# Kernel tuning notes

Hardware: AMD Instinct MI355X
Metric: run time of the kernel (lower is better)

Reference implementation:

```python
import jax, jax.numpy as jnp
import numpy as np

C = 512
GROUPS = 8
EPS = 1e-5


def setup_inputs() -> dict:
    key = jax.random.key(0)
    ks = jax.random.split(key, 7)
    B, H, W = 16, 32, 32
    x = jax.random.normal(ks[0], (B, C, H, W), dtype=jnp.float32)
    gamma = jnp.ones((C,), jnp.float32)
    beta = jnp.zeros((C,), jnp.float32)
    # 1x1 convs stored as [out, in] matrices
    w_qkv = jax.random.normal(ks[1], (3 * C, C), dtype=jnp.float32) * (1.0 / np.sqrt(C))
    b_qkv = jax.random.normal(ks[2], (3 * C,), dtype=jnp.float32) * 0.02
    w_proj = jax.random.normal(ks[3], (C, C), dtype=jnp.float32) * (1.0 / np.sqrt(C))
    b_proj = jax.random.normal(ks[4], (C,), dtype=jnp.float32) * 0.02
    return {"x": x, "gamma": gamma, "beta": beta, "w_qkv": w_qkv,
            "b_qkv": b_qkv, "w_proj": w_proj, "b_proj": b_proj}


def _group_norm(x, gamma, beta):
    B, Cc, H, W = x.shape
    xg = x.reshape(B, GROUPS, Cc // GROUPS, H, W)
    mean = xg.mean(axis=(2, 3, 4), keepdims=True)
    var = xg.var(axis=(2, 3, 4), keepdims=True)
    xg = (xg - mean) * jax.lax.rsqrt(var + EPS)
    x = xg.reshape(B, Cc, H, W)
    return x * gamma[None, :, None, None] + beta[None, :, None, None]


def reference(x, gamma, beta, w_qkv, b_qkv, w_proj, b_proj):
    B, Cc, H, W = x.shape
    N = H * W
    h = _group_norm(x, gamma, beta)  # [B,C,H,W]
    hf = h.reshape(B, Cc, N)  # [B,C,N]
    # 1x1 conv == matmul over channel dim
    qkv = jnp.einsum('oc,bcn->bon', w_qkv, hf) + b_qkv[None, :, None]  # [B,3C,N]
    q, k, v = jnp.split(qkv, 3, axis=1)  # each [B,C,N]
    scale = 1.0 / jnp.sqrt(jnp.float32(Cc))
    # attn[b,i,j] = sum_c q[b,c,i] * k[b,c,j]
    attn = jnp.einsum('bci,bcj->bij', q, k) * scale  # [B,N,N]
    attn = jax.nn.softmax(attn, axis=-1)
    out = jnp.einsum('bij,bcj->bci', attn, v)  # [B,C,N]
    out = jnp.einsum('oc,bcn->bon', w_proj, out) + b_proj[None, :, None]
    return x + out.reshape(B, Cc, H, W)
```

## Files before the change

### kernel.cpp

```cpp
#include <hip/hip_runtime.h>
#include <hip/hip_bf16.h>

typedef unsigned short u16;
typedef unsigned int u32;
typedef __attribute__((ext_vector_type(8))) short short8;
typedef __attribute__((ext_vector_type(4))) float floatx4;

#define BATCH 16
#define CDIM 512
#define NSPAT 1024
#define NGROUP 8

__device__ __forceinline__ u16 f2bf(float f) {
    unsigned u = __float_as_uint(f);
    u += 0x7FFFu + ((u >> 16) & 1u);
    return (u16)(u >> 16);
}
__device__ __forceinline__ u32 f2bf2(float lo, float hi) {
    __hip_bfloat162 h = __float22bfloat162_rn(make_float2(lo, hi));
    return *(u32*)&h;
}

__device__ __forceinline__ void load_lds16(const void* g, void* l) {
    __builtin_amdgcn_global_load_lds(
        (const __attribute__((address_space(1))) unsigned int*)g,
        (__attribute__((address_space(3))) unsigned int*)l, 16, 0, 0);
}

__global__ __launch_bounds__(256) void prep_kernel(
    const float* __restrict__ w_qkv, const float* __restrict__ w_proj,
    const float* __restrict__ b_qkv, const float* __restrict__ x,
    u16* __restrict__ wmega, u16* __restrict__ wproj_bf, u16* __restrict__ wv_t,
    float* __restrict__ stats, float* __restrict__ lsums, float* __restrict__ bpv) {
    int b = blockIdx.x;
    int tid = threadIdx.x;
    if (b < 768) {
        const float* src = (b < 512) ? w_qkv : w_proj;
        u16* dst = (b < 512) ? wmega : wproj_bf;
        int i = (b < 512 ? b : b - 512) * 256 + tid;
        float4 v = ((const float4*)src)[i];
        u32* d = (u32*)dst;
        d[i * 2] = f2bf2(v.x, v.y);
        d[i * 2 + 1] = f2bf2(v.z, v.w);
        return;
    }
    if (b < 832) {
        __shared__ u16 t[64 * 66];
        int bt = b - 768;
        int tx = bt & 7, ty = bt >> 3;
        const float* src = w_qkv + (size_t)(1024 + ty * 64) * CDIM + tx * 64;
#pragma unroll
        for (int p = 0; p < 4; ++p) {
            int r = p * 16 + (tid >> 4);
            int c4 = (tid & 15) << 2;
            float4 v = *(const float4*)(src + (size_t)r * CDIM + c4);
            u16* d = &t[r * 66 + c4];
            d[0] = f2bf(v.x); d[1] = f2bf(v.y); d[2] = f2bf(v.z); d[3] = f2bf(v.w);
        }
        __syncthreads();
        u16* dst = wv_t + (size_t)(tx * 64) * CDIM + ty * 64;
#pragma unroll
        for (int p = 0; p < 4; ++p) {
            int c = p * 16 + (tid >> 4);
            int r4 = (tid & 15) << 2;
            ushort4 o;
            o.x = t[(r4 + 0) * 66 + c];
            o.y = t[(r4 + 1) * 66 + c];
            o.z = t[(r4 + 2) * 66 + c];
            o.w = t[(r4 + 3) * 66 + c];
            *(ushort4*)(dst + (size_t)c * CDIM + r4) = o;
        }
        return;
    }
    if (b < 960) {
        __shared__ float rs[4], rss[4];
        int bg = b - 832;
        const float4* xv = (const float4*)(x + (size_t)bg * 65536);
        float s = 0.f, ss = 0.f;
        for (int i = tid; i < 16384; i += 256) {
            float4 v = xv[i];
            s += v.x + v.y + v.z + v.w;
            ss += v.x * v.x + v.y * v.y + v.z * v.z + v.w * v.w;
        }
#pragma unroll
        for (int off = 32; off; off >>= 1) { s += __shfl_down(s, off); ss += __shfl_down(ss, off); }
        int wave = tid >> 6, lane = tid & 63;
        if (lane == 0) { rs[wave] = s; rss[wave] = ss; }
        __syncthreads();
        if (tid == 0) {
            float S1 = rs[0] + rs[1] + rs[2] + rs[3];
            float S2 = rss[0] + rss[1] + rss[2] + rss[3];
            float mean = S1 * (1.f / 65536.f);
            float var = S2 * (1.f / 65536.f) - mean * mean;
            stats[bg * 2] = mean;
            stats[bg * 2 + 1] = rsqrtf(var + 1e-5f);
        }
        return;
    }
    if (b < 976) {
        ((float4*)lsums)[(b - 960) * 256 + tid] = (float4){0.f, 0.f, 0.f, 0.f};
        return;
    }
    {
        int o0 = (b - 976) * 64;
        int wave = tid >> 6, lane = tid & 63;
        const float4* bvv = (const float4*)(b_qkv + 1024);
        float4 v0 = bvv[lane * 2], v1 = bvv[lane * 2 + 1];
        for (int it = 0; it < 16; ++it) {
            int o = o0 + wave * 16 + it;
            const float4* wr = (const float4*)(w_proj + (size_t)o * CDIM);
            float4 a0 = wr[lane * 2], a1 = wr[lane * 2 + 1];
            float s = a0.x * v0.x + a0.y * v0.y + a0.z * v0.z + a0.w * v0.w
                    + a1.x * v1.x + a1.y * v1.y + a1.z * v1.z + a1.w * v1.w;
#pragma unroll
            for (int off = 32; off; off >>= 1) s += __shfl_down(s, off);
            if (lane == 0) bpv[o] = s;
        }
    }
}

__device__ __forceinline__ void stage_tile(
    const u16* __restrict__ Ab, const u16* __restrict__ Bb, int lda, int ldb,
    int m0, int n0, int k0, u16* As, u16* Bs) {
    int tid = threadIdx.x;
#pragma unroll
    for (int it = 0; it < 4; ++it) {
        int c = it * 256 + tid;
        int r = c >> 3, p = c & 7;
        int kc = p ^ (r & 7);
        load_lds16(Ab + (size_t)(m0 + r) * lda + k0 + (kc << 3), &As[c << 3]);
        load_lds16(Bb + (size_t)(n0 + r) * ldb + k0 + (kc << 3), &Bs[c << 3]);
    }
}

__device__ __forceinline__ void compute_tile(
    const u16* As, const u16* Bs, int wm, int wn, int quad, int lrow,
    floatx4 (&acc)[4][4]) {
#pragma unroll
    for (int s = 0; s < 2; ++s) {
        short8 af[4], bf[4];
#pragma unroll
        for (int i = 0; i < 4; ++i) {
            int R = wm + i * 16 + lrow;
            int p = (s * 4 + quad) ^ (R & 7);
            af[i] = *(const short8*)&As[(R << 6) + (p << 3)];
        }
#pragma unroll
        for (int j = 0; j < 4; ++j) {
            int R = wn + j * 16 + lrow;
            int p = (s * 4 + quad) ^ (R & 7);
            bf[j] = *(const short8*)&Bs[(R << 6) + (p << 3)];
        }
#pragma unroll
        for (int i = 0; i < 4; ++i)
#pragma unroll
            for (int j = 0; j < 4; ++j)
                acc[i][j] = __builtin_amdgcn_mfma_f32_16x16x32_bf16(af[i], bf[j], acc[i][j], 0, 0, 0);
    }
}

template <bool DB>
__device__ __forceinline__ void gemm_core(
    const u16* __restrict__ Ab, const u16* __restrict__ Bb, int K, int lda, int ldb,
    int m0, int n0, u16* As, u16* Bs, floatx4 (&acc)[4][4]) {
    int tid = threadIdx.x;
    int lane = tid & 63, wave = tid >> 6, quad = lane >> 4, lrow = lane & 15;
    int wm = (wave >> 1) << 6, wn = (wave & 1) << 6;
    if constexpr (!DB) {
        for (int k0 = 0; k0 < K; k0 += 64) {
            stage_tile(Ab, Bb, lda, ldb, m0, n0, k0, As, Bs);
            __syncthreads();
            compute_tile(As, Bs, wm, wn, quad, lrow, acc);
            __syncthreads();
        }
    } else {
        const int TS = 128 * 64;
        int nt = K >> 6;
        stage_tile(Ab, Bb, lda, ldb, m0, n0, 0, As, Bs);
        u16 *Ac = As, *Bc = Bs, *An = As + TS, *Bn = Bs + TS;
        for (int t = 0; t < nt - 1; ++t) {
            stage_tile(Ab, Bb, lda, ldb, m0, n0, (t + 1) << 6, An, Bn);
            asm volatile("s_waitcnt vmcnt(8)" ::: "memory");
            __builtin_amdgcn_s_barrier();
            __builtin_amdgcn_sched_barrier(0);
            compute_tile(Ac, Bc, wm, wn, quad, lrow, acc);
            __builtin_amdgcn_sched_barrier(0);
            __builtin_amdgcn_s_barrier();
            u16* t0 = Ac; Ac = An; An = t0;
            u16* t1 = Bc; Bc = Bn; Bn = t1;
        }
        asm volatile("s_waitcnt vmcnt(0)" ::: "memory");
        __builtin_amdgcn_s_barrier();
        __builtin_amdgcn_sched_barrier(0);
        compute_tile(Ac, Bc, wm, wn, quad, lrow, acc);
    }
}

#define ACC_INIT floatx4 acc[4][4]; \
    _Pragma("unroll") for (int i = 0; i < 4; ++i) \
    _Pragma("unroll") for (int j = 0; j < 4; ++j) acc[i][j] = (floatx4){0.f, 0.f, 0.f, 0.f};

#define EPILOG_IDX int lane = threadIdx.x & 63, wave = threadIdx.x >> 6; \
    int quad = lane >> 4, lrow = lane & 15; \
    int wm = (wave >> 1) << 6, wn = (wave & 1) << 6;

#define TSTR 66
__global__ __launch_bounds__(256) void gn_wpv_kernel(
    const float* __restrict__ x, const float* __restrict__ gamma, const float* __restrict__ beta,
    const float* __restrict__ stats, u16* __restrict__ hT,
    const u16* __restrict__ wproj_bf, const u16* __restrict__ wv_t, u16* __restrict__ wmega) {
    __shared__ u16 smem[2 * 128 * 64];
    int tid = threadIdx.x;
    if (blockIdx.z == 16) {
        if (blockIdx.x >= 4 || blockIdx.y >= 4) return;
        int m0 = blockIdx.y << 7, n0 = blockIdx.x << 7;
        ACC_INIT;
        gemm_core<false>(wproj_bf, wv_t, CDIM, CDIM, CDIM, m0, n0, smem, smem + 128 * 64, acc);
        EPILOG_IDX;
#pragma unroll
        for (int i = 0; i < 4; ++i)
#pragma unroll
            for (int j = 0; j < 4; ++j)
#pragma unroll
                for (int r = 0; r < 4; ++r) {
                    int R = m0 + wm + i * 16 + (quad << 2) + r;
                    int Cc = n0 + wn + j * 16 + lrow;
                    wmega[(size_t)(1024 + R) * CDIM + Cc] = f2bf(acc[i][j][r]);
                }
        return;
    }
    u16* t = smem;
    int b = blockIdx.z, c0 = blockIdx.y << 6, n0 = blockIdx.x << 6;
    const float* xb = x + ((size_t)b * CDIM + c0) * NSPAT + n0;
#pragma unroll
    for (int p = 0; p < 4; ++p) {
        int cl = p * 16 + (tid >> 4);
        int nl = (tid & 15) << 2;
        int c = c0 + cl;
        int bg = b * NGROUP + (c >> 6);
        float ga = gamma[c] * stats[bg * 2 + 1];
        float be = beta[c] - stats[bg * 2] * ga;
        float4 v = *(const float4*)(xb + (size_t)cl * NSPAT + nl);
        u16* dst = &t[cl * TSTR + nl];
        dst[0] = f2bf(v.x * ga + be);
        dst[1] = f2bf(v.y * ga + be);
        dst[2] = f2bf(v.z * ga + be);
        dst[3] = f2bf(v.w * ga + be);
    }
    __syncthreads();
    u16* hb = hT + ((size_t)b * NSPAT + n0) * CDIM + c0;
#pragma unroll
    for (int p = 0; p < 4; ++p) {
        int nl = p * 16 + (tid >> 4);
        int cl4 = (tid & 15) << 2;
        ushort4 o;
        o.x = t[(cl4 + 0) * TSTR + nl];
        o.y = t[(cl4 + 1) * TSTR + nl];
        o.z = t[(cl4 + 2) * TSTR + nl];
        o.w = t[(cl4 + 3) * TSTR + nl];
        *(ushort4*)(hb + (size_t)nl * CDIM + cl4) = o;
    }
}

__global__ __launch_bounds__(256) void qkv_kernel(
    const u16* __restrict__ wmega, const u16* __restrict__ hT,
    const float* __restrict__ b_qkv, const float* __restrict__ bpv,
    u16* __restrict__ qkT, u16* __restrict__ WV) {
    __shared__ u16 As[2 * 128 * 64];
    __shared__ u16 Bs[2 * 128 * 64];
    int z = blockIdx.x;
    int n0 = blockIdx.y << 7;
    int m0 = blockIdx.z << 7;
    const u16* Bb = hT + (size_t)z * CDIM * NSPAT;
    ACC_INIT;
    gemm_core<true>(wmega, Bb, CDIM, CDIM, CDIM, m0, n0, As, Bs, acc);
    EPILOG_IDX;
    if (blockIdx.z < 8) {
        u16* qk = qkT + (size_t)z * NSPAT * NSPAT;
#pragma unroll
        for (int i = 0; i < 4; ++i)
#pragma unroll
            for (int j = 0; j < 4; ++j) {
                int R0 = m0 + wm + i * 16 + (quad << 2);
                int Cc = n0 + wn + j * 16 + lrow;
                uint2 u;
                u.x = f2bf2(acc[i][j][0] + b_qkv[R0 + 0], acc[i][j][1] + b_qkv[R0 + 1]);
                u.y = f2bf2(acc[i][j][2] + b_qkv[R0 + 2], acc[i][j][3] + b_qkv[R0 + 3]);
                *(uint2*)&qk[(size_t)Cc * NSPAT + R0] = u;
            }
    } else {
        u16* Wp = WV + (size_t)z * CDIM * NSPAT;
#pragma unroll
        for (int i = 0; i < 4; ++i)
#pragma unroll
            for (int j = 0; j < 4; ++j)
#pragma unroll
                for (int r = 0; r < 4; ++r) {
                    int R = m0 - 1024 + wm + i * 16 + (quad << 2) + r;
                    int Cc = n0 + wn + j * 16 + lrow;
                    Wp[(size_t)R * NSPAT + Cc] = f2bf(acc[i][j][r] + bpv[R]);
                }
    }
}

__global__ __launch_bounds__(256) void scores_kernel(
    const u16* __restrict__ qkT, u16* __restrict__ P, float* __restrict__ lsums, float scale) {
    __shared__ u16 As[2 * 128 * 64];
    __shared__ u16 Bs[2 * 128 * 64];
    int z = blockIdx.x;
    int n0 = blockIdx.y << 7;
    int m0 = blockIdx.z << 7;
    const u16* qb = qkT + (size_t)z * NSPAT * NSPAT;
    ACC_INIT;
    gemm_core<true>(qb + CDIM, qb, CDIM, NSPAT, NSPAT, m0, n0, As, Bs, acc);
    EPILOG_IDX;
    u16* Pp = P + (size_t)z * NSPAT * NSPAT;
    float* ls = lsums + (size_t)z * NSPAT;
#pragma unroll
    for (int nj = 0; nj < 4; ++nj) {
        int Ci = n0 + wn + nj * 16 + lrow;
        float part = 0.f;
#pragma unroll
        for (int mi = 0; mi < 4; ++mi) {
            int Rj0 = m0 + wm + mi * 16 + (quad << 2);
            float e0 = __expf(acc[mi][nj][0] * scale);
            float e1 = __expf(acc[mi][nj][1] * scale);
            float e2 = __expf(acc[mi][nj][2] * scale);
            float e3 = __expf(acc[mi][nj][3] * scale);
            part += (e0 + e1) + (e2 + e3);
            uint2 u;
            u.x = f2bf2(e0, e1);
            u.y = f2bf2(e2, e3);
            *(uint2*)&Pp[(size_t)Ci * NSPAT + Rj0] = u;
        }
        part += __shfl_xor(part, 16);
        part += __shfl_xor(part, 32);
        if (lane < 16) atomicAdd(&ls[Ci], part);
    }
}

__global__ __launch_bounds__(256) void final_kernel(
    const u16* __restrict__ WV, const u16* __restrict__ P, const float* __restrict__ lsums,
    const float* __restrict__ bias, const float* __restrict__ x, float* __restrict__ out) {
    __shared__ u16 As[2 * 128 * 64];
    __shared__ u16 Bs[2 * 128 * 64];
    int z = blockIdx.x;
    int n0 = blockIdx.y << 7;
    int m0 = blockIdx.z << 7;
    const u16* Pb = P + (size_t)z * NSPAT * NSPAT;
    const u16* WVb = WV + (size_t)z * CDIM * NSPAT;
    ACC_INIT;
    gemm_core<true>(Pb, WVb, NSPAT, NSPAT, NSPAT, m0, n0, As, Bs, acc);
    EPILOG_IDX;
    float* Op = out + (size_t)z * CDIM * NSPAT;
    const float* xr = x + (size_t)z * CDIM * NSPAT;
    const float* li = lsums + (size_t)z * NSPAT;
#pragma unroll
    for (int mi = 0; mi < 4; ++mi) {
        int Ri0 = m0 + wm + mi * 16 + (quad << 2);
        float4 lv = *(const float4*)&li[Ri0];
        float s0 = __builtin_amdgcn_rcpf(lv.x);
        float s1 = __builtin_amdgcn_rcpf(lv.y);
        float s2 = __builtin_amdgcn_rcpf(lv.z);
        float s3 = __builtin_amdgcn_rcpf(lv.w);
#pragma unroll
        for (int nj = 0; nj < 4; ++nj) {
            int Co = n0 + wn + nj * 16 + lrow;
            float bv = bias[Co];
            size_t off = (size_t)Co * NSPAT + Ri0;
            float4 xv = *(const float4*)&xr[off];
            float4 o;
            o.x = acc[mi][nj][0] * s0 + bv + xv.x;
            o.y = acc[mi][nj][1] * s1 + bv + xv.y;
            o.z = acc[mi][nj][2] * s2 + bv + xv.z;
            o.w = acc[mi][nj][3] * s3 + bv + xv.w;
            *(float4*)&Op[off] = o;
        }
    }
}

extern "C" void kernel_launch(void* const* d_in, const int* in_sizes, int n_in,
                              void* d_out, int out_size, void* d_ws, size_t ws_size,
                              hipStream_t stream) {
    const float* x      = (const float*)d_in[0];
    const float* gamma  = (const float*)d_in[1];
    const float* beta   = (const float*)d_in[2];
    const float* w_qkv  = (const float*)d_in[3];
    const float* b_qkv  = (const float*)d_in[4];
    const float* w_proj = (const float*)d_in[5];
    const float* b_proj = (const float*)d_in[6];
    float* out = (float*)d_out;

    const size_t CN = (size_t)CDIM * NSPAT;
    const size_t NN = (size_t)NSPAT * NSPAT;
    const float SCALE = 0.044194173824159216f;

    char* ws = (char*)d_ws;
    float* stats   = (float*)ws;
    float* bpv     = (float*)(ws + 1024);
    u16* wmega     = (u16*)(ws + 4096);
    u16* wproj_bf  = wmega + (size_t)3 * CDIM * CDIM;
    u16* wv_t      = wproj_bf + (size_t)CDIM * CDIM;
    u16* hT        = wv_t + (size_t)CDIM * CDIM;
    u16* qkT       = hT + BATCH * CN;
    u16* WV        = qkT + BATCH * NN;
    u16* P         = WV + BATCH * CN;
    float* lsums   = (float*)(P + BATCH * NN);

    prep_kernel<<<984, 256, 0, stream>>>(
        w_qkv, w_proj, b_qkv, x, wmega, wproj_bf, wv_t, stats, lsums, bpv);

    gn_wpv_kernel<<<dim3(16, 8, 17), 256, 0, stream>>>(
        x, gamma, beta, stats, hT, wproj_bf, wv_t, wmega);

    qkv_kernel<<<dim3(BATCH, 8, 12), 256, 0, stream>>>(
        wmega, hT, b_qkv, bpv, qkT, WV);

    scores_kernel<<<dim3(BATCH, 8, 8), 256, 0, stream>>>(qkT, P, lsums, SCALE);

    final_kernel<<<dim3(BATCH, 4, 8), 256, 0, stream>>>(WV, P, lsums, b_proj, x, out);
}
```

Baseline: 142.8 us.

## Load A operand fragments directly from global into registers, staging only B in LDS

The three main GEMM kernels no longer stage the A tile in shared memory. Each wave loads its A fragments straight from global memory into registers, double-buffered across k-steps, while B stays double-buffered in LDS. This halves LDS footprint and LDS traffic per block and may raise occupancy. In exchange, A rows are read from global by both waves that share an M half, so there is redundant global/L2 traffic, lanes issue uncoalesced 16-byte loads, and register pressure rises from the extra fragment buffers.

```diff
diff --git a/kernel.cpp b/kernel.cpp
--- a/kernel.cpp
+++ b/kernel.cpp
@@ -159,41 +159,88 @@
     }
 }
 
-template <bool DB>
-__device__ __forceinline__ void gemm_core(
+__device__ __forceinline__ void gemm_core_sb(
     const u16* __restrict__ Ab, const u16* __restrict__ Bb, int K, int lda, int ldb,
     int m0, int n0, u16* As, u16* Bs, floatx4 (&acc)[4][4]) {
     int tid = threadIdx.x;
     int lane = tid & 63, wave = tid >> 6, quad = lane >> 4, lrow = lane & 15;
     int wm = (wave >> 1) << 6, wn = (wave & 1) << 6;
-    if constexpr (!DB) {
-        for (int k0 = 0; k0 < K; k0 += 64) {
-            stage_tile(Ab, Bb, lda, ldb, m0, n0, k0, As, Bs);
-            __syncthreads();
-            compute_tile(As, Bs, wm, wn, quad, lrow, acc);
-            __syncthreads();
-        }
-    } else {
-        const int TS = 128 * 64;
-        int nt = K >> 6;
-        stage_tile(Ab, Bb, lda, ldb, m0, n0, 0, As, Bs);
-        u16 *Ac = As, *Bc = Bs, *An = As + TS, *Bn = Bs + TS;
-        for (int t = 0; t < nt - 1; ++t) {
-            stage_tile(Ab, Bb, lda, ldb, m0, n0, (t + 1) << 6, An, Bn);
-            asm volatile("s_waitcnt vmcnt(8)" ::: "memory");
-            __builtin_amdgcn_s_barrier();
-            __builtin_amdgcn_sched_barrier(0);
-            compute_tile(Ac, Bc, wm, wn, quad, lrow, acc);
-            __builtin_amdgcn_sched_barrier(0);
-            __builtin_amdgcn_s_barrier();
-            u16* t0 = Ac; Ac = An; An = t0;
-            u16* t1 = Bc; Bc = Bn; Bn = t1;
-        }
-        asm volatile("s_waitcnt vmcnt(0)" ::: "memory");
+    for (int k0 = 0; k0 < K; k0 += 64) {
+        stage_tile(Ab, Bb, lda, ldb, m0, n0, k0, As, Bs);
+        __syncthreads();
+        compute_tile(As, Bs, wm, wn, quad, lrow, acc);
+        __syncthreads();
+    }
+}
+
+__device__ __forceinline__ void stage_B(
+    const u16* __restrict__ Bb, int ldb, int n0, int k0, u16* Bs) {
+    int tid = threadIdx.x;
+#pragma unroll
+    for (int it = 0; it < 4; ++it) {
+        int c = it * 256 + tid;
+        int r = c >> 3, p = c & 7;
+        int kc = p ^ (r & 7);
+        load_lds16(Bb + (size_t)(n0 + r) * ldb + k0 + (kc << 3), &Bs[c << 3]);
+    }
+}
+
+#define LOAD_AFRAG(dst, base, lda, k0) \
+    _Pragma("unroll") for (int i_ = 0; i_ < 4; ++i_) \
+    _Pragma("unroll") for (int s_ = 0; s_ < 2; ++s_) \
+        dst[s_ * 4 + i_] = *(const short8*)((base) + (size_t)i_ * 16 * (lda) + (k0) + s_ * 32);
+
+__device__ __forceinline__ void compute_ra(
+    const short8 (&af)[8], const u16* Bs, int wn, int quad, int lrow,
+    floatx4 (&acc)[4][4]) {
+#pragma unroll
+    for (int s = 0; s < 2; ++s) {
+        short8 bf[4];
+#pragma unroll
+        for (int j = 0; j < 4; ++j) {
+            int R = wn + j * 16 + lrow;
+            int p = (s * 4 + quad) ^ (R & 7);
+            bf[j] = *(const short8*)&Bs[(R << 6) + (p << 3)];
+        }
+#pragma unroll
+        for (int i = 0; i < 4; ++i)
+#pragma unroll
+            for (int j = 0; j < 4; ++j)
+                acc[i][j] = __builtin_amdgcn_mfma_f32_16x16x32_bf16(af[s * 4 + i], bf[j], acc[i][j], 0, 0, 0);
+    }
+}
+
+__device__ __forceinline__ void gemm_core_ra(
+    const u16* __restrict__ Ab, const u16* __restrict__ Bb, int K, int lda, int ldb,
+    int m0, int n0, u16* Bs, floatx4 (&acc)[4][4]) {
+    int tid = threadIdx.x;
+    int lane = tid & 63, wave = tid >> 6, quad = lane >> 4, lrow = lane & 15;
+    int wn = (wave & 1) << 6;
+    int wm = (wave >> 1) << 6;
+    const u16* ap = Ab + (size_t)(m0 + wm + lrow) * lda + (quad << 3);
+    const int TS = 128 * 64;
+    int nt = K >> 6;
+    short8 afc[8], afn[8];
+    stage_B(Bb, ldb, n0, 0, Bs);
+    LOAD_AFRAG(afc, ap, lda, 0);
+    u16 *Bc = Bs, *Bn = Bs + TS;
+    for (int t = 0; t < nt - 1; ++t) {
+        stage_B(Bb, ldb, n0, (t + 1) << 6, Bn);
+        LOAD_AFRAG(afn, ap, lda, (t + 1) << 6);
+        asm volatile("s_waitcnt vmcnt(12)" ::: "memory");
         __builtin_amdgcn_s_barrier();
         __builtin_amdgcn_sched_barrier(0);
-        compute_tile(Ac, Bc, wm, wn, quad, lrow, acc);
-    }
+        compute_ra(afc, Bc, wn, quad, lrow, acc);
+        __builtin_amdgcn_sched_barrier(0);
+        __builtin_amdgcn_s_barrier();
+#pragma unroll
+        for (int i = 0; i < 8; ++i) afc[i] = afn[i];
+        u16* tb = Bc; Bc = Bn; Bn = tb;
+    }
+    asm volatile("s_waitcnt vmcnt(0)" ::: "memory");
+    __builtin_amdgcn_s_barrier();
+    __builtin_amdgcn_sched_barrier(0);
+    compute_ra(afc, Bc, wn, quad, lrow, acc);
 }
 
 #define ACC_INIT floatx4 acc[4][4]; \
@@ -215,7 +262,7 @@
         if (blockIdx.x >= 4 || blockIdx.y >= 4) return;
         int m0 = blockIdx.y << 7, n0 = blockIdx.x << 7;
         ACC_INIT;
-        gemm_core<false>(wproj_bf, wv_t, CDIM, CDIM, CDIM, m0, n0, smem, smem + 128 * 64, acc);
+        gemm_core_sb(wproj_bf, wv_t, CDIM, CDIM, CDIM, m0, n0, smem, smem + 128 * 64, acc);
         EPILOG_IDX;
 #pragma unroll
         for (int i = 0; i < 4; ++i)
@@ -266,14 +313,13 @@
     const u16* __restrict__ wmega, const u16* __restrict__ hT,
     const float* __restrict__ b_qkv, const float* __restrict__ bpv,
     u16* __restrict__ qkT, u16* __restrict__ WV) {
-    __shared__ u16 As[2 * 128 * 64];
     __shared__ u16 Bs[2 * 128 * 64];
     int z = blockIdx.x;
     int n0 = blockIdx.y << 7;
     int m0 = blockIdx.z << 7;
     const u16* Bb = hT + (size_t)z * CDIM * NSPAT;
     ACC_INIT;
-    gemm_core<true>(wmega, Bb, CDIM, CDIM, CDIM, m0, n0, As, Bs, acc);
+    gemm_core_ra(wmega, Bb, CDIM, CDIM, CDIM, m0, n0, Bs, acc);
     EPILOG_IDX;
     if (blockIdx.z < 8) {
         u16* qk = qkT + (size_t)z * NSPAT * NSPAT;
@@ -305,14 +351,13 @@
 
 __global__ __launch_bounds__(256) void scores_kernel(
     const u16* __restrict__ qkT, u16* __restrict__ P, float* __restrict__ lsums, float scale) {
-    __shared__ u16 As[2 * 128 * 64];
     __shared__ u16 Bs[2 * 128 * 64];
     int z = blockIdx.x;
     int n0 = blockIdx.y << 7;
     int m0 = blockIdx.z << 7;
     const u16* qb = qkT + (size_t)z * NSPAT * NSPAT;
     ACC_INIT;
-    gemm_core<true>(qb + CDIM, qb, CDIM, NSPAT, NSPAT, m0, n0, As, Bs, acc);
+    gemm_core_ra(qb + CDIM, qb, CDIM, NSPAT, NSPAT, m0, n0, Bs, acc);
     EPILOG_IDX;
     u16* Pp = P + (size_t)z * NSPAT * NSPAT;
     float* ls = lsums + (size_t)z * NSPAT;
@@ -342,7 +387,6 @@
 __global__ __launch_bounds__(256) void final_kernel(
     const u16* __restrict__ WV, const u16* __restrict__ P, const float* __restrict__ lsums,
     const float* __restrict__ bias, const float* __restrict__ x, float* __restrict__ out) {
-    __shared__ u16 As[2 * 128 * 64];
     __shared__ u16 Bs[2 * 128 * 64];
     int z = blockIdx.x;
     int n0 = blockIdx.y << 7;
@@ -350,7 +394,7 @@
     const u16* Pb = P + (size_t)z * NSPAT * NSPAT;
     const u16* WVb = WV + (size_t)z * CDIM * NSPAT;
     ACC_INIT;
-    gemm_core<true>(Pb, WVb, NSPAT, NSPAT, NSPAT, m0, n0, As, Bs, acc);
+    gemm_core_ra(Pb, WVb, NSPAT, NSPAT, NSPAT, m0, n0, Bs, acc);
     EPILOG_IDX;
     float* Op = out + (size_t)z * CDIM * NSPAT;
     const float* xr = x + (size_t)z * CDIM * NSPAT;
```

Result: slower. 194.7 us (+36.3%).
